# Kernel tuning notes

Measured on AMD Instinct MI355X. Metric: run time of the kernel, lower is better.

Reference implementation:

```python
import jax, jax.numpy as jnp
import numpy as np

N = 100_000
E = 3_200_000
FEAT, HID, EMB = 128, 32, 16
NEG_SLOPE = 0.2


def setup_inputs() -> dict:
    key = jax.random.key(0)
    ks = jax.random.split(key, 12)
    x = jax.random.normal(ks[0], (N, FEAT), dtype=jnp.float32)
    ei = jax.random.randint(ks[1], (2, E), 0, N, dtype=jnp.int32)
    ew = jax.random.uniform(ks[2], (E, 1), dtype=jnp.float32)
    # GATConv layer 1: feat_dim -> hidden_dim, heads=1
    s1 = 1.0 / np.sqrt(FEAT)
    W1 = jax.random.normal(ks[3], (FEAT, HID), dtype=jnp.float32) * s1
    a_src1 = jax.random.normal(ks[4], (HID,), dtype=jnp.float32) * (1.0 / np.sqrt(HID))
    a_dst1 = jax.random.normal(ks[5], (HID,), dtype=jnp.float32) * (1.0 / np.sqrt(HID))
    b1 = jnp.zeros((HID,), dtype=jnp.float32)
    # GATConv layer 2: hidden_dim -> embed_dim, heads=1
    s2 = 1.0 / np.sqrt(HID)
    W2 = jax.random.normal(ks[6], (HID, EMB), dtype=jnp.float32) * s2
    a_src2 = jax.random.normal(ks[7], (EMB,), dtype=jnp.float32) * (1.0 / np.sqrt(EMB))
    a_dst2 = jax.random.normal(ks[8], (EMB,), dtype=jnp.float32) * (1.0 / np.sqrt(EMB))
    b2 = jnp.zeros((EMB,), dtype=jnp.float32)
    return {"x": x, "ei": ei, "ew": ew, "W1": W1, "a_src1": a_src1,
            "a_dst1": a_dst1, "b1": b1, "W2": W2, "a_src2": a_src2,
            "a_dst2": a_dst2, "b2": b2}


def gat_conv(x, src, dst, W, a_src, a_dst, b):
    """PyG GATConv, heads=1, add_self_loops=True, edge_attr ignored (edge_dim=None)."""
    n = x.shape[0]
    h = x @ W                              # [N, C]
    al_s = h @ a_src                       # [N]
    al_d = h @ a_dst                       # [N]
    loop = jnp.arange(n, dtype=src.dtype)
    srcs = jnp.concatenate([src, loop])    # [E+N]
    dsts = jnp.concatenate([dst, loop])
    alpha = jax.nn.leaky_relu(al_s[srcs] + al_d[dsts], NEG_SLOPE)
    # segment softmax over edges grouped by destination node
    m = jax.ops.segment_max(alpha, dsts, num_segments=n)
    e = jnp.exp(alpha - m[dsts])
    denom = jax.ops.segment_sum(e, dsts, num_segments=n)
    coef = e / (denom[dsts] + 1e-16)
    out = jax.ops.segment_sum(coef[:, None] * h[srcs], dsts, num_segments=n)
    return out + b


def reference(x, ei, ew, W1, a_src1, a_dst1, b1, W2, a_src2, a_dst2, b2):
    # eval mode: DropEdge and Dropout are identity; ew unused by GATConv (edge_dim=None)
    src, dst = ei[0], ei[1]
    h = gat_conv(x, src, dst, W1, a_src1, a_dst1, b1)
    h = jax.nn.relu(h)
    return gat_conv(h, src, dst, W2, a_src2, a_dst2, b2)
```

## Files before the change

kernel.cpp:

```cpp
#include <hip/hip_runtime.h>

#define FEAT 128
#define HID 32
#define EMB 16
#define NEG 0.2f

#define BSH 8
#define BIN_NODES 256
#define NBMAX 400
#define CH 8192
#define CAP 12288
#define SRCBITS 17
#define SRCMASK 0x1FFFF

__device__ __forceinline__ float lrelu(float a) { return a > 0.0f ? a : NEG * a; }

__global__ __launch_bounds__(256) void k_zero_int(int* p, int n) {
    int i = (int)(blockIdx.x * 256 + threadIdx.x);
    if (i < n) p[i] = 0;
}

__global__ __launch_bounds__(256) void k_bincnt(const int* __restrict__ ei, int E_,
                                                int Nn, int* __restrict__ binCnt) {
    __shared__ int h[NBMAX];
    int nb = (Nn + BIN_NODES - 1) >> BSH;
    for (int i = threadIdx.x; i < nb; i += 256) h[i] = 0;
    __syncthreads();
    int stride = (int)(gridDim.x * 256);
    for (int i = (int)(blockIdx.x * 256 + threadIdx.x); i < E_; i += stride)
        atomicAdd(&h[ei[(size_t)E_ + i] >> BSH], 1);
    __syncthreads();
    for (int i = threadIdx.x; i < nb; i += 256)
        if (h[i]) atomicAdd(&binCnt[i], h[i]);
}

__global__ __launch_bounds__(512) void k_binscan(const int* __restrict__ binCnt,
                                                 int* __restrict__ binstart,
                                                 int* __restrict__ bin_pos,
                                                 int* __restrict__ rowptr,
                                                 int Nn, int E_) {
    __shared__ int s[512];
    int nb = (Nn + BIN_NODES - 1) >> BSH;
    int t = (int)threadIdx.x;
    s[t] = (t < nb) ? binCnt[t] : 0;
    __syncthreads();
    for (int off = 1; off < 512; off <<= 1) {
        int v = (t >= off) ? s[t - off] : 0;
        __syncthreads();
        s[t] += v;
        __syncthreads();
    }
    if (t <= nb) binstart[t] = (t == 0) ? 0 : s[t - 1];
    if (t < nb) bin_pos[t] = (t == 0) ? 0 : s[t - 1];
    if (t == 0) rowptr[Nn] = E_;
}

__global__ __launch_bounds__(1024) void k_part(const int* __restrict__ ei, int E_,
                                               int Nn, int* __restrict__ bin_pos,
                                               int* __restrict__ packed) {
    __shared__ int hist[NBMAX];
    __shared__ int lofs[NBMAX];
    __shared__ int pos[NBMAX];
    __shared__ int gbase[NBMAX];
    __shared__ int sscan[512];
    __shared__ int staged[CH];
    __shared__ unsigned short sbin[CH];
    int nb = (Nn + BIN_NODES - 1) >> BSH;
    int base = (int)(blockIdx.x * CH);
    int nE = min(CH, E_ - base);
    int t = (int)threadIdx.x;
    for (int i = t; i < nb; i += 1024) hist[i] = 0;
    __syncthreads();

    int myw[CH / 1024];
    int myb[CH / 1024];
#pragma unroll
    for (int k = 0; k < CH / 1024; ++k) {
        int i = t + k * 1024;
        int w = 0, b_ = -1;
        if (i < nE) {
            int s_ = ei[base + i];
            int d_ = ei[(size_t)E_ + base + i];
            b_ = d_ >> BSH;
            w = ((d_ & (BIN_NODES - 1)) << SRCBITS) | s_;
            atomicAdd(&hist[b_], 1);
        }
        myw[k] = w;
        myb[k] = b_;
    }
    __syncthreads();
    if (t < 512) sscan[t] = (t < nb) ? hist[t] : 0;
    __syncthreads();
    for (int off = 1; off < 512; off <<= 1) {
        int v = 0;
        if (t < 512 && t >= off) v = sscan[t - off];
        __syncthreads();
        if (t < 512) sscan[t] += v;
        __syncthreads();
    }
    for (int i = t; i < nb; i += 1024) {
        int ex = (i == 0) ? 0 : sscan[i - 1];
        lofs[i] = ex;
        pos[i] = ex;
    }
    __syncthreads();
#pragma unroll
    for (int k = 0; k < CH / 1024; ++k) {
        if (myb[k] >= 0) {
            int p = atomicAdd(&pos[myb[k]], 1);
            staged[p] = myw[k];
            sbin[p] = (unsigned short)myb[k];
        }
    }
    __syncthreads();
    for (int i = t; i < nb; i += 1024)
        gbase[i] = hist[i] ? atomicAdd(&bin_pos[i], hist[i]) : 0;
    __syncthreads();
    for (int i = t; i < nE; i += 1024) {
        int b_ = sbin[i];
        packed[gbase[b_] + (i - lofs[b_])] = staged[i];
    }
}

__global__ __launch_bounds__(1024) void k_build(const int* __restrict__ binstart,
                                                int Nn, int E_,
                                                int* __restrict__ packed,
                                                int* __restrict__ rowptr,
                                                int* __restrict__ scratch) {
    __shared__ int ncnt[BIN_NODES];
    __shared__ int npos[BIN_NODES];
    __shared__ int sscan[BIN_NODES];
    __shared__ int csr_l[CAP];
    int b = (int)blockIdx.x;
    int s = binstart[b], e = binstart[b + 1];
    int cnt = e - s;
    int nb0 = b << BSH;
    int nodes = min(BIN_NODES, Nn - nb0);
    int t = (int)threadIdx.x;
    if (t < BIN_NODES) ncnt[t] = 0;
    __syncthreads();
    for (int i = t; i < cnt; i += 1024) atomicAdd(&ncnt[packed[s + i] >> SRCBITS], 1);
    __syncthreads();
    if (t < BIN_NODES) sscan[t] = ncnt[t];
    __syncthreads();
    for (int off = 1; off < BIN_NODES; off <<= 1) {
        int v = 0;
        if (t < BIN_NODES && t >= off) v = sscan[t - off];
        __syncthreads();
        if (t < BIN_NODES) sscan[t] += v;
        __syncthreads();
    }
    if (t < BIN_NODES) {
        int ex = (t == 0) ? 0 : sscan[t - 1];
        npos[t] = ex;
        if (t < nodes) rowptr[nb0 + t] = s + ex;
    }
    __syncthreads();
    if (cnt <= CAP) {
        for (int i = t; i < cnt; i += 1024) {
            int w = packed[s + i];
            int p = atomicAdd(&npos[w >> SRCBITS], 1);
            csr_l[p] = w & SRCMASK;
        }
        __syncthreads();
        for (int i = t; i < cnt; i += 1024) packed[s + i] = csr_l[i];
    } else {
        for (int i = t; i < cnt; i += 1024) scratch[s + i] = packed[s + i];
        __syncthreads();
        for (int i = t; i < cnt; i += 1024) {
            int w = scratch[s + i];
            int p = atomicAdd(&npos[w >> SRCBITS], 1);
            packed[s + p] = w & SRCMASK;
        }
    }
}

__global__ __launch_bounds__(256) void k_h1(
    const float* __restrict__ x, const float* __restrict__ W1,
    const float* __restrict__ a_s, const float* __restrict__ a_d,
    float* __restrict__ h1, float* __restrict__ als, float* __restrict__ ald, int Nn)
{
    int row = (int)(blockIdx.x * 256 + threadIdx.x);
    if (row >= Nn) return;
    const float4* xr = (const float4*)(x + (size_t)row * FEAT);
    float acc[HID];
#pragma unroll
    for (int c = 0; c < HID; ++c) acc[c] = 0.0f;
#pragma unroll 4
    for (int k4 = 0; k4 < FEAT / 4; ++k4) {
        float4 xv = xr[k4];
        const float* Wr = W1 + k4 * 4 * HID;
#pragma unroll
        for (int c = 0; c < HID; ++c)
            acc[c] += xv.x * Wr[c] + xv.y * Wr[HID + c]
                    + xv.z * Wr[2 * HID + c] + xv.w * Wr[3 * HID + c];
    }
    float4* hr = (float4*)(h1 + (size_t)row * HID);
    float ps = 0.0f, pd = 0.0f;
#pragma unroll
    for (int c4 = 0; c4 < HID / 4; ++c4) {
        float4 hv;
        hv.x = acc[4 * c4 + 0]; hv.y = acc[4 * c4 + 1];
        hv.z = acc[4 * c4 + 2]; hv.w = acc[4 * c4 + 3];
        hr[c4] = hv;
        ps += hv.x * a_s[4 * c4 + 0] + hv.y * a_s[4 * c4 + 1]
            + hv.z * a_s[4 * c4 + 2] + hv.w * a_s[4 * c4 + 3];
        pd += hv.x * a_d[4 * c4 + 0] + hv.y * a_d[4 * c4 + 1]
            + hv.z * a_d[4 * c4 + 2] + hv.w * a_d[4 * c4 + 3];
    }
    als[row] = ps;
    ald[row] = pd;
}

__global__ __launch_bounds__(256) void k_agg1(
    const int* __restrict__ rowptr, const int* __restrict__ csr_src,
    const float* __restrict__ h1, const float* __restrict__ als,
    const float* __restrict__ ald, const float* __restrict__ b1,
    const float* __restrict__ W2, const float* __restrict__ a_s2,
    const float* __restrict__ a_d2,
    float* __restrict__ h2, float* __restrict__ als2, float* __restrict__ ald2, int Nn)
{
    int n = (int)(blockIdx.x * 32 + (threadIdx.x >> 3));
    if (n >= Nn) return;
    int l = threadIdx.x & 7;
    const float4* h1p = (const float4*)h1;
    float aldn = ald[n];
    float wself = __expf(lrelu(als[n] + aldn));
    float4 sv = h1p[(size_t)n * 8 + l];
    float s0x = wself * sv.x, s0y = wself * sv.y;
    float s0z = wself * sv.z, s0w = wself * sv.w;
    float s1x = 0, s1y = 0, s1z = 0, s1w = 0;
    float s2x = 0, s2y = 0, s2z = 0, s2w = 0;
    float s3x = 0, s3y = 0, s3z = 0, s3w = 0;
    float den = wself;
    int e = rowptr[n], e1 = rowptr[n + 1];
    for (; e + 4 <= e1; e += 4) {
        int i0 = csr_src[e + 0];
        int i1 = csr_src[e + 1];
        int i2 = csr_src[e + 2];
        int i3 = csr_src[e + 3];
        float4 f0 = h1p[(size_t)i0 * 8 + l];
        float4 f1 = h1p[(size_t)i1 * 8 + l];
        float4 f2 = h1p[(size_t)i2 * 8 + l];
        float4 f3 = h1p[(size_t)i3 * 8 + l];
        float a0 = als[i0], a1 = als[i1], a2 = als[i2], a3 = als[i3];
        float w0 = __expf(lrelu(a0 + aldn));
        float w1 = __expf(lrelu(a1 + aldn));
        float w2 = __expf(lrelu(a2 + aldn));
        float w3 = __expf(lrelu(a3 + aldn));
        s0x += w0 * f0.x; s0y += w0 * f0.y; s0z += w0 * f0.z; s0w += w0 * f0.w;
        s1x += w1 * f1.x; s1y += w1 * f1.y; s1z += w1 * f1.z; s1w += w1 * f1.w;
        s2x += w2 * f2.x; s2y += w2 * f2.y; s2z += w2 * f2.z; s2w += w2 * f2.w;
        s3x += w3 * f3.x; s3y += w3 * f3.y; s3z += w3 * f3.z; s3w += w3 * f3.w;
        den += (w0 + w1) + (w2 + w3);
    }
    for (; e < e1; ++e) {
        int s = csr_src[e];
        float we = __expf(lrelu(als[s] + aldn));
        float4 f = h1p[(size_t)s * 8 + l];
        s0x += we * f.x; s0y += we * f.y; s0z += we * f.z; s0w += we * f.w;
        den += we;
    }
    float inv = 1.0f / den;
    float gx = fmaxf((s0x + s1x + s2x + s3x) * inv + b1[4 * l + 0], 0.0f);
    float gy = fmaxf((s0y + s1y + s2y + s3y) * inv + b1[4 * l + 1], 0.0f);
    float gz = fmaxf((s0z + s1z + s2z + s3z) * inv + b1[4 * l + 2], 0.0f);
    float gw = fmaxf((s0w + s1w + s2w + s3w) * inv + b1[4 * l + 3], 0.0f);
    float hc0 = 0.0f, hc1 = 0.0f;
#pragma unroll
    for (int tt = 0; tt < 8; ++tt) {
        float bx = __shfl(gx, tt, 8);
        float by = __shfl(gy, tt, 8);
        float bz = __shfl(gz, tt, 8);
        float bw = __shfl(gw, tt, 8);
        const float* wp = &W2[(4 * tt) * EMB];
        hc0 += bx * wp[l] + by * wp[EMB + l]
             + bz * wp[2 * EMB + l] + bw * wp[3 * EMB + l];
        hc1 += bx * wp[l + 8] + by * wp[EMB + l + 8]
             + bz * wp[2 * EMB + l + 8] + bw * wp[3 * EMB + l + 8];
    }
    h2[(size_t)n * EMB + l] = hc0;
    h2[(size_t)n * EMB + l + 8] = hc1;
    float ps = hc0 * a_s2[l] + hc1 * a_s2[l + 8];
    float pd = hc0 * a_d2[l] + hc1 * a_d2[l + 8];
    for (int m = 1; m < 8; m <<= 1) {
        ps += __shfl_xor(ps, m, 8);
        pd += __shfl_xor(pd, m, 8);
    }
    if (l == 0) { als2[n] = ps; ald2[n] = pd; }
}

__global__ __launch_bounds__(256) void k_agg2(
    const int* __restrict__ rowptr, const int* __restrict__ csr_src,
    const float* __restrict__ h2, const float* __restrict__ als,
    const float* __restrict__ ald, const float* __restrict__ b2,
    float* __restrict__ out, int Nn)
{
    int n = (int)(blockIdx.x * 64 + (threadIdx.x >> 2));
    if (n >= Nn) return;
    int l = threadIdx.x & 3;
    const float4* h2p = (const float4*)h2;
    float aldn = ald[n];
    float wself = __expf(lrelu(als[n] + aldn));
    float4 sv = h2p[(size_t)n * 4 + l];
    float s0x = wself * sv.x, s0y = wself * sv.y;
    float s0z = wself * sv.z, s0w = wself * sv.w;
    float s1x = 0, s1y = 0, s1z = 0, s1w = 0;
    float s2x = 0, s2y = 0, s2z = 0, s2w = 0;
    float s3x = 0, s3y = 0, s3z = 0, s3w = 0;
    float den = wself;
    int e = rowptr[n], e1 = rowptr[n + 1];
    for (; e + 4 <= e1; e += 4) {
        int i0 = csr_src[e + 0];
        int i1 = csr_src[e + 1];
        int i2 = csr_src[e + 2];
        int i3 = csr_src[e + 3];
        float4 f0 = h2p[(size_t)i0 * 4 + l];
        float4 f1 = h2p[(size_t)i1 * 4 + l];
        float4 f2 = h2p[(size_t)i2 * 4 + l];
        float4 f3 = h2p[(size_t)i3 * 4 + l];
        float a0 = als[i0], a1 = als[i1], a2 = als[i2], a3 = als[i3];
        float w0 = __expf(lrelu(a0 + aldn));
        float w1 = __expf(lrelu(a1 + aldn));
        float w2 = __expf(lrelu(a2 + aldn));
        float w3 = __expf(lrelu(a3 + aldn));
        s0x += w0 * f0.x; s0y += w0 * f0.y; s0z += w0 * f0.z; s0w += w0 * f0.w;
        s1x += w1 * f1.x; s1y += w1 * f1.y; s1z += w1 * f1.z; s1w += w1 * f1.w;
        s2x += w2 * f2.x; s2y += w2 * f2.y; s2z += w2 * f2.z; s2w += w2 * f2.w;
        s3x += w3 * f3.x; s3y += w3 * f3.y; s3z += w3 * f3.z; s3w += w3 * f3.w;
        den += (w0 + w1) + (w2 + w3);
    }
    for (; e < e1; ++e) {
        int s = csr_src[e];
        float we = __expf(lrelu(als[s] + aldn));
        float4 f = h2p[(size_t)s * 4 + l];
        s0x += we * f.x; s0y += we * f.y; s0z += we * f.z; s0w += we * f.w;
        den += we;
    }
    float inv = 1.0f / den;
    float4 r;
    r.x = (s0x + s1x + s2x + s3x) * inv + b2[4 * l + 0];
    r.y = (s0y + s1y + s2y + s3y) * inv + b2[4 * l + 1];
    r.z = (s0z + s1z + s2z + s3z) * inv + b2[4 * l + 2];
    r.w = (s0w + s1w + s2w + s3w) * inv + b2[4 * l + 3];
    ((float4*)out)[(size_t)n * 4 + l] = r;
}

extern "C" void kernel_launch(void* const* d_in, const int* in_sizes, int n_in,
                              void* d_out, int out_size, void* d_ws, size_t ws_size,
                              hipStream_t stream)
{
    const float* x   = (const float*)d_in[0];
    const int*   ei  = (const int*)d_in[1];
    const float* W1  = (const float*)d_in[3];
    const float* as1 = (const float*)d_in[4];
    const float* ad1 = (const float*)d_in[5];
    const float* b1  = (const float*)d_in[6];
    const float* W2  = (const float*)d_in[7];
    const float* as2 = (const float*)d_in[8];
    const float* ad2 = (const float*)d_in[9];
    const float* b2  = (const float*)d_in[10];
    float* out = (float*)d_out;

    const int Nn = in_sizes[0] / FEAT;
    const int E_ = in_sizes[1] / 2;
    const int nb = (Nn + BIN_NODES - 1) >> BSH;

    float* h1    = (float*)d_ws;
    float* als1  = h1 + (size_t)Nn * HID;
    float* ald1  = als1 + Nn;
    float* h2    = ald1 + Nn;
    float* als2p = h2 + (size_t)Nn * EMB;
    float* ald2p = als2p + Nn;
    int* rowptr  = (int*)(ald2p + Nn);
    int* binCnt  = rowptr + Nn + 1;
    int* binstart= binCnt + NBMAX;
    int* bin_pos = binstart + NBMAX + 1;
    int* packed  = bin_pos + NBMAX;

    k_zero_int<<<(nb + 255) / 256, 256, 0, stream>>>(binCnt, nb);
    k_bincnt<<<1024, 256, 0, stream>>>(ei, E_, Nn, binCnt);
    k_binscan<<<1, 512, 0, stream>>>(binCnt, binstart, bin_pos, rowptr, Nn, E_);
    k_part<<<(E_ + CH - 1) / CH, 1024, 0, stream>>>(ei, E_, Nn, bin_pos, packed);
    k_build<<<nb, 1024, 0, stream>>>(binstart, Nn, E_, packed, rowptr, (int*)h1);

    k_h1<<<(Nn + 255) / 256, 256, 0, stream>>>(x, W1, as1, ad1, h1, als1, ald1, Nn);
    k_agg1<<<(Nn + 31) / 32, 256, 0, stream>>>(rowptr, packed, h1, als1, ald1,
                                               b1, W2, as2, ad2, h2, als2p, ald2p, Nn);
    k_agg2<<<(Nn + 63) / 64, 256, 0, stream>>>(rowptr, packed, h2, als2p, ald2p,
                                               b2, out, Nn);
}
```

Before: 321.7 us.

## Precompute per-edge attention weights in a separate pass and vectorize CSR reads

The CSR words now keep the local destination index, and a new per-bin kernel uses it to compute the exp(leaky_relu) edge weight for every edge in a coalesced pass, writing them to a workspace buffer. The aggregation kernels then read 4 indices and 4 weights with aligned int4/float4 loads instead of gathering als per edge and evaluating exp inline, after a scalar head loop that brings the edge index to a multiple of 4. Layer 2 aggregation also changes from 4 lanes of float4 to 8 lanes of float2 per node. This adds an extra E-sized write and read per layer plus two more launches, and falls back to the old path when the workspace is too small.

Result: slower. 363.2 us (+12.9%).

```diff
diff --git a/kernel.cpp b/kernel.cpp
--- a/kernel.cpp
+++ b/kernel.cpp
@@ -139,7 +139,7 @@
     int t = (int)threadIdx.x;
     if (t < BIN_NODES) ncnt[t] = 0;
     __syncthreads();
-    for (int i = t; i < cnt; i += 1024) atomicAdd(&ncnt[packed[s + i] >> SRCBITS], 1);
+    for (int i = t; i < cnt; i += 1024) atomicAdd(&ncnt[(packed[s + i] >> SRCBITS) & 255], 1);
     __syncthreads();
     if (t < BIN_NODES) sscan[t] = ncnt[t];
     __syncthreads();
@@ -159,8 +159,8 @@
     if (cnt <= CAP) {
         for (int i = t; i < cnt; i += 1024) {
             int w = packed[s + i];
-            int p = atomicAdd(&npos[w >> SRCBITS], 1);
-            csr_l[p] = w & SRCMASK;
+            int p = atomicAdd(&npos[(w >> SRCBITS) & 255], 1);
+            csr_l[p] = w;
         }
         __syncthreads();
         for (int i = t; i < cnt; i += 1024) packed[s + i] = csr_l[i];
@@ -169,8 +169,8 @@
         __syncthreads();
         for (int i = t; i < cnt; i += 1024) {
             int w = scratch[s + i];
-            int p = atomicAdd(&npos[w >> SRCBITS], 1);
-            packed[s + p] = w & SRCMASK;
+            int p = atomicAdd(&npos[(w >> SRCBITS) & 255], 1);
+            packed[s + p] = w;
         }
     }
 }
@@ -212,8 +212,26 @@
     ald[row] = pd;
 }
 
+__global__ __launch_bounds__(1024) void k_wgt(const int* __restrict__ binstart,
+                                              const int* __restrict__ packed,
+                                              const float* __restrict__ als,
+                                              const float* __restrict__ ald,
+                                              float* __restrict__ wbuf) {
+    int b = (int)blockIdx.x;
+    int s = binstart[b], e = binstart[b + 1];
+    int nb0 = b << BSH;
+    for (int i = s + (int)threadIdx.x; i < e; i += 1024) {
+        int w = packed[i];
+        int src = w & SRCMASK;
+        int d = nb0 + ((w >> SRCBITS) & 255);
+        wbuf[i] = __expf(lrelu(als[src] + ald[d]));
+    }
+}
+
+template<bool HASW>
 __global__ __launch_bounds__(256) void k_agg1(
-    const int* __restrict__ rowptr, const int* __restrict__ csr_src,
+    const int* __restrict__ rowptr, const int* __restrict__ csr,
+    const float* __restrict__ wbuf,
     const float* __restrict__ h1, const float* __restrict__ als,
     const float* __restrict__ ald, const float* __restrict__ b1,
     const float* __restrict__ W2, const float* __restrict__ a_s2,
@@ -234,20 +252,34 @@
     float s3x = 0, s3y = 0, s3z = 0, s3w = 0;
     float den = wself;
     int e = rowptr[n], e1 = rowptr[n + 1];
+    for (; e < e1 && (e & 3); ++e) {
+        int word = csr[e];
+        int s = word & SRCMASK;
+        float we;
+        if constexpr (HASW) we = wbuf[e];
+        else we = __expf(lrelu(als[s] + aldn));
+        float4 f = h1p[(size_t)s * 8 + l];
+        s0x += we * f.x; s0y += we * f.y; s0z += we * f.z; s0w += we * f.w;
+        den += we;
+    }
     for (; e + 4 <= e1; e += 4) {
-        int i0 = csr_src[e + 0];
-        int i1 = csr_src[e + 1];
-        int i2 = csr_src[e + 2];
-        int i3 = csr_src[e + 3];
+        int4 c4 = *(const int4*)(csr + e);
+        int i0 = c4.x & SRCMASK, i1 = c4.y & SRCMASK;
+        int i2 = c4.z & SRCMASK, i3 = c4.w & SRCMASK;
+        float w0, w1, w2, w3;
+        if constexpr (HASW) {
+            float4 w4 = *(const float4*)(wbuf + e);
+            w0 = w4.x; w1 = w4.y; w2 = w4.z; w3 = w4.w;
+        } else {
+            w0 = __expf(lrelu(als[i0] + aldn));
+            w1 = __expf(lrelu(als[i1] + aldn));
+            w2 = __expf(lrelu(als[i2] + aldn));
+            w3 = __expf(lrelu(als[i3] + aldn));
+        }
         float4 f0 = h1p[(size_t)i0 * 8 + l];
         float4 f1 = h1p[(size_t)i1 * 8 + l];
         float4 f2 = h1p[(size_t)i2 * 8 + l];
         float4 f3 = h1p[(size_t)i3 * 8 + l];
-        float a0 = als[i0], a1 = als[i1], a2 = als[i2], a3 = als[i3];
-        float w0 = __expf(lrelu(a0 + aldn));
-        float w1 = __expf(lrelu(a1 + aldn));
-        float w2 = __expf(lrelu(a2 + aldn));
-        float w3 = __expf(lrelu(a3 + aldn));
         s0x += w0 * f0.x; s0y += w0 * f0.y; s0z += w0 * f0.z; s0w += w0 * f0.w;
         s1x += w1 * f1.x; s1y += w1 * f1.y; s1z += w1 * f1.z; s1w += w1 * f1.w;
         s2x += w2 * f2.x; s2y += w2 * f2.y; s2z += w2 * f2.z; s2w += w2 * f2.w;
@@ -255,8 +287,11 @@
         den += (w0 + w1) + (w2 + w3);
     }
     for (; e < e1; ++e) {
-        int s = csr_src[e];
-        float we = __expf(lrelu(als[s] + aldn));
+        int word = csr[e];
+        int s = word & SRCMASK;
+        float we;
+        if constexpr (HASW) we = wbuf[e];
+        else we = __expf(lrelu(als[s] + aldn));
         float4 f = h1p[(size_t)s * 8 + l];
         s0x += we * f.x; s0y += we * f.y; s0z += we * f.z; s0w += we * f.w;
         den += we;
@@ -290,60 +325,74 @@
     if (l == 0) { als2[n] = ps; ald2[n] = pd; }
 }
 
+template<bool HASW>
 __global__ __launch_bounds__(256) void k_agg2(
-    const int* __restrict__ rowptr, const int* __restrict__ csr_src,
+    const int* __restrict__ rowptr, const int* __restrict__ csr,
+    const float* __restrict__ wbuf,
     const float* __restrict__ h2, const float* __restrict__ als,
     const float* __restrict__ ald, const float* __restrict__ b2,
     float* __restrict__ out, int Nn)
 {
-    int n = (int)(blockIdx.x * 64 + (threadIdx.x >> 2));
+    int n = (int)(blockIdx.x * 32 + (threadIdx.x >> 3));
     if (n >= Nn) return;
-    int l = threadIdx.x & 3;
-    const float4* h2p = (const float4*)h2;
+    int l = threadIdx.x & 7;
+    const float2* h2p = (const float2*)h2;
     float aldn = ald[n];
     float wself = __expf(lrelu(als[n] + aldn));
-    float4 sv = h2p[(size_t)n * 4 + l];
+    float2 sv = h2p[(size_t)n * 8 + l];
     float s0x = wself * sv.x, s0y = wself * sv.y;
-    float s0z = wself * sv.z, s0w = wself * sv.w;
-    float s1x = 0, s1y = 0, s1z = 0, s1w = 0;
-    float s2x = 0, s2y = 0, s2z = 0, s2w = 0;
-    float s3x = 0, s3y = 0, s3z = 0, s3w = 0;
+    float s1x = 0, s1y = 0, s2x = 0, s2y = 0, s3x = 0, s3y = 0;
     float den = wself;
     int e = rowptr[n], e1 = rowptr[n + 1];
+    for (; e < e1 && (e & 3); ++e) {
+        int word = csr[e];
+        int s = word & SRCMASK;
+        float we;
+        if constexpr (HASW) we = wbuf[e];
+        else we = __expf(lrelu(als[s] + aldn));
+        float2 f = h2p[(size_t)s * 8 + l];
+        s0x += we * f.x; s0y += we * f.y;
+        den += we;
+    }
     for (; e + 4 <= e1; e += 4) {
-        int i0 = csr_src[e + 0];
-        int i1 = csr_src[e + 1];
-        int i2 = csr_src[e + 2];
-        int i3 = csr_src[e + 3];
-        float4 f0 = h2p[(size_t)i0 * 4 + l];
-        float4 f1 = h2p[(size_t)i1 * 4 + l];
-        float4 f2 = h2p[(size_t)i2 * 4 + l];
-        float4 f3 = h2p[(size_t)i3 * 4 + l];
-        float a0 = als[i0], a1 = als[i1], a2 = als[i2], a3 = als[i3];
-        float w0 = __expf(lrelu(a0 + aldn));
-        float w1 = __expf(lrelu(a1 + aldn));
-        float w2 = __expf(lrelu(a2 + aldn));
-        float w3 = __expf(lrelu(a3 + aldn));
-        s0x += w0 * f0.x; s0y += w0 * f0.y; s0z += w0 * f0.z; s0w += w0 * f0.w;
-        s1x += w1 * f1.x; s1y += w1 * f1.y; s1z += w1 * f1.z; s1w += w1 * f1.w;
-        s2x += w2 * f2.x; s2y += w2 * f2.y; s2z += w2 * f2.z; s2w += w2 * f2.w;
-        s3x += w3 * f3.x; s3y += w3 * f3.y; s3z += w3 * f3.z; s3w += w3 * f3.w;
+        int4 c4 = *(const int4*)(csr + e);
+        int i0 = c4.x & SRCMASK, i1 = c4.y & SRCMASK;
+        int i2 = c4.z & SRCMASK, i3 = c4.w & SRCMASK;
+        float w0, w1, w2, w3;
+        if constexpr (HASW) {
+            float4 w4 = *(const float4*)(wbuf + e);
+            w0 = w4.x; w1 = w4.y; w2 = w4.z; w3 = w4.w;
+        } else {
+            w0 = __expf(lrelu(als[i0] + aldn));
+            w1 = __expf(lrelu(als[i1] + aldn));
+            w2 = __expf(lrelu(als[i2] + aldn));
+            w3 = __expf(lrelu(als[i3] + aldn));
+        }
+        float2 f0 = h2p[(size_t)i0 * 8 + l];
+        float2 f1 = h2p[(size_t)i1 * 8 + l];
+        float2 f2 = h2p[(size_t)i2 * 8 + l];
+        float2 f3 = h2p[(size_t)i3 * 8 + l];
+        s0x += w0 * f0.x; s0y += w0 * f0.y;
+        s1x += w1 * f1.x; s1y += w1 * f1.y;
+        s2x += w2 * f2.x; s2y += w2 * f2.y;
+        s3x += w3 * f3.x; s3y += w3 * f3.y;
         den += (w0 + w1) + (w2 + w3);
     }
     for (; e < e1; ++e) {
-        int s = csr_src[e];
-        float we = __expf(lrelu(als[s] + aldn));
-        float4 f = h2p[(size_t)s * 4 + l];
-        s0x += we * f.x; s0y += we * f.y; s0z += we * f.z; s0w += we * f.w;
+        int word = csr[e];
+        int s = word & SRCMASK;
+        float we;
+        if constexpr (HASW) we = wbuf[e];
+        else we = __expf(lrelu(als[s] + aldn));
+        float2 f = h2p[(size_t)s * 8 + l];
+        s0x += we * f.x; s0y += we * f.y;
         den += we;
     }
     float inv = 1.0f / den;
-    float4 r;
-    r.x = (s0x + s1x + s2x + s3x) * inv + b2[4 * l + 0];
-    r.y = (s0y + s1y + s2y + s3y) * inv + b2[4 * l + 1];
-    r.z = (s0z + s1z + s2z + s3z) * inv + b2[4 * l + 2];
-    r.w = (s0w + s1w + s2w + s3w) * inv + b2[4 * l + 3];
-    ((float4*)out)[(size_t)n * 4 + l] = r;
+    float2 r;
+    r.x = (s0x + s1x + s2x + s3x) * inv + b2[2 * l];
+    r.y = (s0y + s1y + s2y + s3y) * inv + b2[2 * l + 1];
+    ((float2*)out)[(size_t)n * 8 + l] = r;
 }
 
 extern "C" void kernel_launch(void* const* d_in, const int* in_sizes, int n_in,
@@ -376,7 +425,11 @@
     int* binCnt  = rowptr + Nn + 1;
     int* binstart= binCnt + NBMAX;
     int* bin_pos = binstart + NBMAX + 1;
-    int* packed  = bin_pos + NBMAX;
+    int* packedr = bin_pos + NBMAX;
+    int* packed  = (int*)(((uintptr_t)packedr + 15) & ~(uintptr_t)15);
+    float* wbuf  = (float*)(packed + E_);
+    size_t need  = (size_t)((char*)(wbuf + E_) - (char*)d_ws);
+    bool hasw    = ws_size >= need;
 
     k_zero_int<<<(nb + 255) / 256, 256, 0, stream>>>(binCnt, nb);
     k_bincnt<<<1024, 256, 0, stream>>>(ei, E_, Nn, binCnt);
@@ -385,8 +438,17 @@
     k_build<<<nb, 1024, 0, stream>>>(binstart, Nn, E_, packed, rowptr, (int*)h1);
 
     k_h1<<<(Nn + 255) / 256, 256, 0, stream>>>(x, W1, as1, ad1, h1, als1, ald1, Nn);
-    k_agg1<<<(Nn + 31) / 32, 256, 0, stream>>>(rowptr, packed, h1, als1, ald1,
-                                               b1, W2, as2, ad2, h2, als2p, ald2p, Nn);
-    k_agg2<<<(Nn + 63) / 64, 256, 0, stream>>>(rowptr, packed, h2, als2p, ald2p,
-                                               b2, out, Nn);
-}
+    if (hasw) {
+        k_wgt<<<nb, 1024, 0, stream>>>(binstart, packed, als1, ald1, wbuf);
+        k_agg1<true><<<(Nn + 31) / 32, 256, 0, stream>>>(rowptr, packed, wbuf,
+            h1, als1, ald1, b1, W2, as2, ad2, h2, als2p, ald2p, Nn);
+        k_wgt<<<nb, 1024, 0, stream>>>(binstart, packed, als2p, ald2p, wbuf);
+        k_agg2<true><<<(Nn + 31) / 32, 256, 0, stream>>>(rowptr, packed, wbuf,
+            h2, als2p, ald2p, b2, out, Nn);
+    } else {
+        k_agg1<false><<<(Nn + 31) / 32, 256, 0, stream>>>(rowptr, packed, nullptr,
+            h1, als1, ald1, b1, W2, as2, ad2, h2, als2p, ald2p, Nn);
+        k_agg2<false><<<(Nn + 31) / 32, 256, 0, stream>>>(rowptr, packed, nullptr,
+            h2, als2p, ald2p, b2, out, Nn);
+    }
+}
```

## Store node features in fp16, fuse h1 projection into bin count, simplify CSR build

Applied to the files above, without the earlier changes.

Layer-1 and layer-2 node features are now stored as half precision, which halves the bytes moved by the random gathers in both aggregation kernels. The dense x@W1 projection is merged into the edge bin-count kernel, removing one launch. The CSR build writes to a separate output array instead of sorting in place through LDS or a scratch copy. agg2 now uses 8 lanes per node with half2 loads. The cost is reduced feature precision, extra workspace for the CSR array, and heavier registers in the fused kernel.

Result: faster. 297.6 us (-7.5%).

```diff
diff --git a/kernel.cpp b/kernel.cpp
--- a/kernel.cpp
+++ b/kernel.cpp
@@ -1,4 +1,5 @@
 #include <hip/hip_runtime.h>
+#include <hip/hip_fp16.h>
 
 #define FEAT 128
 #define HID 32
@@ -9,7 +10,6 @@
 #define BIN_NODES 256
 #define NBMAX 400
 #define CH 8192
-#define CAP 12288
 #define SRCBITS 17
 #define SRCMASK 0x1FFFF
 
@@ -20,14 +20,47 @@
     if (i < n) p[i] = 0;
 }
 
-__global__ __launch_bounds__(256) void k_bincnt(const int* __restrict__ ei, int E_,
-                                                int Nn, int* __restrict__ binCnt) {
+__global__ __launch_bounds__(256) void k_bincnt_h1(
+    const int* __restrict__ ei, int E_, int Nn, int* __restrict__ binCnt,
+    const float* __restrict__ x, const float* __restrict__ W1,
+    const float* __restrict__ a_s, const float* __restrict__ a_d,
+    __half* __restrict__ h1h, float* __restrict__ als, float* __restrict__ ald)
+{
     __shared__ int h[NBMAX];
     int nb = (Nn + BIN_NODES - 1) >> BSH;
     for (int i = threadIdx.x; i < nb; i += 256) h[i] = 0;
     __syncthreads();
+    int tid = (int)(blockIdx.x * 256 + threadIdx.x);
+    if (tid < Nn) {
+        const float4* xr = (const float4*)(x + (size_t)tid * FEAT);
+        float acc[HID];
+#pragma unroll
+        for (int c = 0; c < HID; ++c) acc[c] = 0.0f;
+#pragma unroll 4
+        for (int k4 = 0; k4 < FEAT / 4; ++k4) {
+            float4 xv = xr[k4];
+            const float* Wr = W1 + k4 * 4 * HID;
+#pragma unroll
+            for (int c = 0; c < HID; ++c)
+                acc[c] += xv.x * Wr[c] + xv.y * Wr[HID + c]
+                        + xv.z * Wr[2 * HID + c] + xv.w * Wr[3 * HID + c];
+        }
+        float ps = 0.0f, pd = 0.0f;
+        __half hb[HID];
+#pragma unroll
+        for (int c = 0; c < HID; ++c) {
+            ps += acc[c] * a_s[c];
+            pd += acc[c] * a_d[c];
+            hb[c] = __float2half(acc[c]);
+        }
+        int4* dst = (int4*)(h1h + (size_t)tid * HID);
+        const int4* sb = (const int4*)hb;
+        dst[0] = sb[0]; dst[1] = sb[1]; dst[2] = sb[2]; dst[3] = sb[3];
+        als[tid] = ps;
+        ald[tid] = pd;
+    }
     int stride = (int)(gridDim.x * 256);
-    for (int i = (int)(blockIdx.x * 256 + threadIdx.x); i < E_; i += stride)
+    for (int i = tid; i < E_; i += stride)
         atomicAdd(&h[ei[(size_t)E_ + i] >> BSH], 1);
     __syncthreads();
     for (int i = threadIdx.x; i < nb; i += 256)
@@ -123,14 +156,13 @@
 }
 
 __global__ __launch_bounds__(1024) void k_build(const int* __restrict__ binstart,
-                                                int Nn, int E_,
-                                                int* __restrict__ packed,
-                                                int* __restrict__ rowptr,
-                                                int* __restrict__ scratch) {
+                                                int Nn,
+                                                const int* __restrict__ packed,
+                                                int* __restrict__ csr,
+                                                int* __restrict__ rowptr) {
     __shared__ int ncnt[BIN_NODES];
     __shared__ int npos[BIN_NODES];
     __shared__ int sscan[BIN_NODES];
-    __shared__ int csr_l[CAP];
     int b = (int)blockIdx.x;
     int s = binstart[b], e = binstart[b + 1];
     int cnt = e - s;
@@ -139,7 +171,8 @@
     int t = (int)threadIdx.x;
     if (t < BIN_NODES) ncnt[t] = 0;
     __syncthreads();
-    for (int i = t; i < cnt; i += 1024) atomicAdd(&ncnt[packed[s + i] >> SRCBITS], 1);
+    for (int i = t; i < cnt; i += 1024)
+        atomicAdd(&ncnt[(packed[s + i] >> SRCBITS) & 255], 1);
     __syncthreads();
     if (t < BIN_NODES) sscan[t] = ncnt[t];
     __syncthreads();
@@ -156,109 +189,73 @@
         if (t < nodes) rowptr[nb0 + t] = s + ex;
     }
     __syncthreads();
-    if (cnt <= CAP) {
-        for (int i = t; i < cnt; i += 1024) {
-            int w = packed[s + i];
-            int p = atomicAdd(&npos[w >> SRCBITS], 1);
-            csr_l[p] = w & SRCMASK;
-        }
-        __syncthreads();
-        for (int i = t; i < cnt; i += 1024) packed[s + i] = csr_l[i];
-    } else {
-        for (int i = t; i < cnt; i += 1024) scratch[s + i] = packed[s + i];
-        __syncthreads();
-        for (int i = t; i < cnt; i += 1024) {
-            int w = scratch[s + i];
-            int p = atomicAdd(&npos[w >> SRCBITS], 1);
-            packed[s + p] = w & SRCMASK;
-        }
-    }
-}
-
-__global__ __launch_bounds__(256) void k_h1(
-    const float* __restrict__ x, const float* __restrict__ W1,
-    const float* __restrict__ a_s, const float* __restrict__ a_d,
-    float* __restrict__ h1, float* __restrict__ als, float* __restrict__ ald, int Nn)
-{
-    int row = (int)(blockIdx.x * 256 + threadIdx.x);
-    if (row >= Nn) return;
-    const float4* xr = (const float4*)(x + (size_t)row * FEAT);
-    float acc[HID];
-#pragma unroll
-    for (int c = 0; c < HID; ++c) acc[c] = 0.0f;
-#pragma unroll 4
-    for (int k4 = 0; k4 < FEAT / 4; ++k4) {
-        float4 xv = xr[k4];
-        const float* Wr = W1 + k4 * 4 * HID;
-#pragma unroll
-        for (int c = 0; c < HID; ++c)
-            acc[c] += xv.x * Wr[c] + xv.y * Wr[HID + c]
-                    + xv.z * Wr[2 * HID + c] + xv.w * Wr[3 * HID + c];
-    }
-    float4* hr = (float4*)(h1 + (size_t)row * HID);
-    float ps = 0.0f, pd = 0.0f;
-#pragma unroll
-    for (int c4 = 0; c4 < HID / 4; ++c4) {
-        float4 hv;
-        hv.x = acc[4 * c4 + 0]; hv.y = acc[4 * c4 + 1];
-        hv.z = acc[4 * c4 + 2]; hv.w = acc[4 * c4 + 3];
-        hr[c4] = hv;
-        ps += hv.x * a_s[4 * c4 + 0] + hv.y * a_s[4 * c4 + 1]
-            + hv.z * a_s[4 * c4 + 2] + hv.w * a_s[4 * c4 + 3];
-        pd += hv.x * a_d[4 * c4 + 0] + hv.y * a_d[4 * c4 + 1]
-            + hv.z * a_d[4 * c4 + 2] + hv.w * a_d[4 * c4 + 3];
-    }
-    als[row] = ps;
-    ald[row] = pd;
+    for (int i = t; i < cnt; i += 1024) {
+        int w = packed[s + i];
+        int p = atomicAdd(&npos[(w >> SRCBITS) & 255], 1);
+        csr[s + p] = w & SRCMASK;
+    }
 }
 
 __global__ __launch_bounds__(256) void k_agg1(
-    const int* __restrict__ rowptr, const int* __restrict__ csr_src,
-    const float* __restrict__ h1, const float* __restrict__ als,
+    const int* __restrict__ rowptr, const int* __restrict__ csr,
+    const __half* __restrict__ h1h, const float* __restrict__ als,
     const float* __restrict__ ald, const float* __restrict__ b1,
     const float* __restrict__ W2, const float* __restrict__ a_s2,
     const float* __restrict__ a_d2,
-    float* __restrict__ h2, float* __restrict__ als2, float* __restrict__ ald2, int Nn)
+    __half* __restrict__ h2h, float* __restrict__ als2, float* __restrict__ ald2,
+    int Nn)
 {
     int n = (int)(blockIdx.x * 32 + (threadIdx.x >> 3));
     if (n >= Nn) return;
     int l = threadIdx.x & 7;
-    const float4* h1p = (const float4*)h1;
+    const __half* h1b = h1h + 4 * l;
     float aldn = ald[n];
     float wself = __expf(lrelu(als[n] + aldn));
-    float4 sv = h1p[(size_t)n * 8 + l];
-    float s0x = wself * sv.x, s0y = wself * sv.y;
-    float s0z = wself * sv.z, s0w = wself * sv.w;
+    uint2 rs = *(const uint2*)(h1b + (size_t)n * HID);
+    float2 pa = __half22float2(*reinterpret_cast<const __half2*>(&rs.x));
+    float2 pb = __half22float2(*reinterpret_cast<const __half2*>(&rs.y));
+    float s0x = wself * pa.x, s0y = wself * pa.y;
+    float s0z = wself * pb.x, s0w = wself * pb.y;
     float s1x = 0, s1y = 0, s1z = 0, s1w = 0;
     float s2x = 0, s2y = 0, s2z = 0, s2w = 0;
     float s3x = 0, s3y = 0, s3z = 0, s3w = 0;
     float den = wself;
     int e = rowptr[n], e1 = rowptr[n + 1];
     for (; e + 4 <= e1; e += 4) {
-        int i0 = csr_src[e + 0];
-        int i1 = csr_src[e + 1];
-        int i2 = csr_src[e + 2];
-        int i3 = csr_src[e + 3];
-        float4 f0 = h1p[(size_t)i0 * 8 + l];
-        float4 f1 = h1p[(size_t)i1 * 8 + l];
-        float4 f2 = h1p[(size_t)i2 * 8 + l];
-        float4 f3 = h1p[(size_t)i3 * 8 + l];
+        int i0 = csr[e + 0];
+        int i1 = csr[e + 1];
+        int i2 = csr[e + 2];
+        int i3 = csr[e + 3];
+        uint2 g0 = *(const uint2*)(h1b + (size_t)i0 * HID);
+        uint2 g1 = *(const uint2*)(h1b + (size_t)i1 * HID);
+        uint2 g2 = *(const uint2*)(h1b + (size_t)i2 * HID);
+        uint2 g3 = *(const uint2*)(h1b + (size_t)i3 * HID);
         float a0 = als[i0], a1 = als[i1], a2 = als[i2], a3 = als[i3];
         float w0 = __expf(lrelu(a0 + aldn));
         float w1 = __expf(lrelu(a1 + aldn));
         float w2 = __expf(lrelu(a2 + aldn));
         float w3 = __expf(lrelu(a3 + aldn));
-        s0x += w0 * f0.x; s0y += w0 * f0.y; s0z += w0 * f0.z; s0w += w0 * f0.w;
-        s1x += w1 * f1.x; s1y += w1 * f1.y; s1z += w1 * f1.z; s1w += w1 * f1.w;
-        s2x += w2 * f2.x; s2y += w2 * f2.y; s2z += w2 * f2.z; s2w += w2 * f2.w;
-        s3x += w3 * f3.x; s3y += w3 * f3.y; s3z += w3 * f3.z; s3w += w3 * f3.w;
+        float2 f0a = __half22float2(*reinterpret_cast<const __half2*>(&g0.x));
+        float2 f0b = __half22float2(*reinterpret_cast<const __half2*>(&g0.y));
+        float2 f1a = __half22float2(*reinterpret_cast<const __half2*>(&g1.x));
+        float2 f1b = __half22float2(*reinterpret_cast<const __half2*>(&g1.y));
+        float2 f2a = __half22float2(*reinterpret_cast<const __half2*>(&g2.x));
+        float2 f2b = __half22float2(*reinterpret_cast<const __half2*>(&g2.y));
+        float2 f3a = __half22float2(*reinterpret_cast<const __half2*>(&g3.x));
+        float2 f3b = __half22float2(*reinterpret_cast<const __half2*>(&g3.y));
+        s0x += w0 * f0a.x; s0y += w0 * f0a.y; s0z += w0 * f0b.x; s0w += w0 * f0b.y;
+        s1x += w1 * f1a.x; s1y += w1 * f1a.y; s1z += w1 * f1b.x; s1w += w1 * f1b.y;
+        s2x += w2 * f2a.x; s2y += w2 * f2a.y; s2z += w2 * f2b.x; s2w += w2 * f2b.y;
+        s3x += w3 * f3a.x; s3y += w3 * f3a.y; s3z += w3 * f3b.x; s3w += w3 * f3b.y;
         den += (w0 + w1) + (w2 + w3);
     }
     for (; e < e1; ++e) {
-        int s = csr_src[e];
+        int s = csr[e];
         float we = __expf(lrelu(als[s] + aldn));
-        float4 f = h1p[(size_t)s * 8 + l];
-        s0x += we * f.x; s0y += we * f.y; s0z += we * f.z; s0w += we * f.w;
+        uint2 g = *(const uint2*)(h1b + (size_t)s * HID);
+        float2 fa = __half22float2(*reinterpret_cast<const __half2*>(&g.x));
+        float2 fb = __half22float2(*reinterpret_cast<const __half2*>(&g.y));
+        s0x += we * fa.x; s0y += we * fa.y; s0z += we * fb.x; s0w += we * fb.y;
         den += we;
     }
     float inv = 1.0f / den;
@@ -279,8 +276,8 @@
         hc1 += bx * wp[l + 8] + by * wp[EMB + l + 8]
              + bz * wp[2 * EMB + l + 8] + bw * wp[3 * EMB + l + 8];
     }
-    h2[(size_t)n * EMB + l] = hc0;
-    h2[(size_t)n * EMB + l + 8] = hc1;
+    h2h[(size_t)n * EMB + l]     = __float2half(hc0);
+    h2h[(size_t)n * EMB + l + 8] = __float2half(hc1);
     float ps = hc0 * a_s2[l] + hc1 * a_s2[l + 8];
     float pd = hc0 * a_d2[l] + hc1 * a_d2[l + 8];
     for (int m = 1; m < 8; m <<= 1) {
@@ -291,59 +288,54 @@
 }
 
 __global__ __launch_bounds__(256) void k_agg2(
-    const int* __restrict__ rowptr, const int* __restrict__ csr_src,
-    const float* __restrict__ h2, const float* __restrict__ als,
+    const int* __restrict__ rowptr, const int* __restrict__ csr,
+    const __half* __restrict__ h2h, const float* __restrict__ als,
     const float* __restrict__ ald, const float* __restrict__ b2,
     float* __restrict__ out, int Nn)
 {
-    int n = (int)(blockIdx.x * 64 + (threadIdx.x >> 2));
+    int n = (int)(blockIdx.x * 32 + (threadIdx.x >> 3));
     if (n >= Nn) return;
-    int l = threadIdx.x & 3;
-    const float4* h2p = (const float4*)h2;
+    int l = threadIdx.x & 7;
+    const __half* h2b = h2h + 2 * l;
     float aldn = ald[n];
     float wself = __expf(lrelu(als[n] + aldn));
-    float4 sv = h2p[(size_t)n * 4 + l];
+    float2 sv = __half22float2(*(const __half2*)(h2b + (size_t)n * EMB));
     float s0x = wself * sv.x, s0y = wself * sv.y;
-    float s0z = wself * sv.z, s0w = wself * sv.w;
-    float s1x = 0, s1y = 0, s1z = 0, s1w = 0;
-    float s2x = 0, s2y = 0, s2z = 0, s2w = 0;
-    float s3x = 0, s3y = 0, s3z = 0, s3w = 0;
+    float s1x = 0, s1y = 0, s2x = 0, s2y = 0, s3x = 0, s3y = 0;
     float den = wself;
     int e = rowptr[n], e1 = rowptr[n + 1];
     for (; e + 4 <= e1; e += 4) {
-        int i0 = csr_src[e + 0];
-        int i1 = csr_src[e + 1];
-        int i2 = csr_src[e + 2];
-        int i3 = csr_src[e + 3];
-        float4 f0 = h2p[(size_t)i0 * 4 + l];
-        float4 f1 = h2p[(size_t)i1 * 4 + l];
-        float4 f2 = h2p[(size_t)i2 * 4 + l];
-        float4 f3 = h2p[(size_t)i3 * 4 + l];
+        int i0 = csr[e + 0];
+        int i1 = csr[e + 1];
+        int i2 = csr[e + 2];
+        int i3 = csr[e + 3];
+        float2 f0 = __half22float2(*(const __half2*)(h2b + (size_t)i0 * EMB));
+        float2 f1 = __half22float2(*(const __half2*)(h2b + (size_t)i1 * EMB));
+        float2 f2 = __half22float2(*(const __half2*)(h2b + (size_t)i2 * EMB));
+        float2 f3 = __half22float2(*(const __half2*)(h2b + (size_t)i3 * EMB));
         float a0 = als[i0], a1 = als[i1], a2 = als[i2], a3 = als[i3];
         float w0 = __expf(lrelu(a0 + aldn));
         float w1 = __expf(lrelu(a1 + aldn));
         float w2 = __expf(lrelu(a2 + aldn));
         float w3 = __expf(lrelu(a3 + aldn));
-        s0x += w0 * f0.x; s0y += w0 * f0.y; s0z += w0 * f0.z; s0w += w0 * f0.w;
-        s1x += w1 * f1.x; s1y += w1 * f1.y; s1z += w1 * f1.z; s1w += w1 * f1.w;
-        s2x += w2 * f2.x; s2y += w2 * f2.y; s2z += w2 * f2.z; s2w += w2 * f2.w;
-        s3x += w3 * f3.x; s3y += w3 * f3.y; s3z += w3 * f3.z; s3w += w3 * f3.w;
+        s0x += w0 * f0.x; s0y += w0 * f0.y;
+        s1x += w1 * f1.x; s1y += w1 * f1.y;
+        s2x += w2 * f2.x; s2y += w2 * f2.y;
+        s3x += w3 * f3.x; s3y += w3 * f3.y;
         den += (w0 + w1) + (w2 + w3);
     }
     for (; e < e1; ++e) {
-        int s = csr_src[e];
+        int s = csr[e];
         float we = __expf(lrelu(als[s] + aldn));
-        float4 f = h2p[(size_t)s * 4 + l];
-        s0x += we * f.x; s0y += we * f.y; s0z += we * f.z; s0w += we * f.w;
+        float2 f = __half22float2(*(const __half2*)(h2b + (size_t)s * EMB));
+        s0x += we * f.x; s0y += we * f.y;
         den += we;
     }
     float inv = 1.0f / den;
-    float4 r;
-    r.x = (s0x + s1x + s2x + s3x) * inv + b2[4 * l + 0];
-    r.y = (s0y + s1y + s2y + s3y) * inv + b2[4 * l + 1];
-    r.z = (s0z + s1z + s2z + s3z) * inv + b2[4 * l + 2];
-    r.w = (s0w + s1w + s2w + s3w) * inv + b2[4 * l + 3];
-    ((float4*)out)[(size_t)n * 4 + l] = r;
+    float2 r;
+    r.x = (s0x + s1x + s2x + s3x) * inv + b2[2 * l];
+    r.y = (s0y + s1y + s2y + s3y) * inv + b2[2 * l + 1];
+    *(float2*)(out + (size_t)n * EMB + 2 * l) = r;
 }
 
 extern "C" void kernel_launch(void* const* d_in, const int* in_sizes, int n_in,
@@ -366,27 +358,31 @@
     const int E_ = in_sizes[1] / 2;
     const int nb = (Nn + BIN_NODES - 1) >> BSH;
 
-    float* h1    = (float*)d_ws;
-    float* als1  = h1 + (size_t)Nn * HID;
-    float* ald1  = als1 + Nn;
-    float* h2    = ald1 + Nn;
-    float* als2p = h2 + (size_t)Nn * EMB;
-    float* ald2p = als2p + Nn;
-    int* rowptr  = (int*)(ald2p + Nn);
-    int* binCnt  = rowptr + Nn + 1;
-    int* binstart= binCnt + NBMAX;
-    int* bin_pos = binstart + NBMAX + 1;
-    int* packed  = bin_pos + NBMAX;
+    __half* h1h   = (__half*)d_ws;
+    float* als1   = (float*)(h1h + (size_t)Nn * HID);
+    float* ald1   = als1 + Nn;
+    __half* h2h   = (__half*)(ald1 + Nn);
+    float* als2p  = (float*)(h2h + (size_t)Nn * EMB);
+    float* ald2p  = als2p + Nn;
+    int* rowptr   = (int*)(ald2p + Nn);
+    int* binCnt   = rowptr + Nn + 1;
+    int* binstart = binCnt + NBMAX;
+    int* bin_pos  = binstart + NBMAX + 1;
+    int* packed   = bin_pos + NBMAX;
+    int* csr      = packed + E_;
 
     k_zero_int<<<(nb + 255) / 256, 256, 0, stream>>>(binCnt, nb);
-    k_bincnt<<<1024, 256, 0, stream>>>(ei, E_, Nn, binCnt);
+    int gb1 = (Nn + 255) / 256;
+    if (gb1 < 1024) gb1 = 1024;
+    k_bincnt_h1<<<gb1, 256, 0, stream>>>(ei, E_, Nn, binCnt,
+                                         x, W1, as1, ad1, h1h, als1, ald1);
     k_binscan<<<1, 512, 0, stream>>>(binCnt, binstart, bin_pos, rowptr, Nn, E_);
     k_part<<<(E_ + CH - 1) / CH, 1024, 0, stream>>>(ei, E_, Nn, bin_pos, packed);
-    k_build<<<nb, 1024, 0, stream>>>(binstart, Nn, E_, packed, rowptr, (int*)h1);
-
-    k_h1<<<(Nn + 255) / 256, 256, 0, stream>>>(x, W1, as1, ad1, h1, als1, ald1, Nn);
-    k_agg1<<<(Nn + 31) / 32, 256, 0, stream>>>(rowptr, packed, h1, als1, ald1,
-                                               b1, W2, as2, ad2, h2, als2p, ald2p, Nn);
-    k_agg2<<<(Nn + 63) / 64, 256, 0, stream>>>(rowptr, packed, h2, als2p, ald2p,
+    k_build<<<nb, 1024, 0, stream>>>(binstart, Nn, packed, csr, rowptr);
+
+    k_agg1<<<(Nn + 31) / 32, 256, 0, stream>>>(rowptr, csr, h1h, als1, ald1,
+                                               b1, W2, as2, ad2,
+                                               h2h, als2p, ald2p, Nn);
+    k_agg2<<<(Nn + 31) / 32, 256, 0, stream>>>(rowptr, csr, h2h, als2p, ald2p,
                                                b2, out, Nn);
 }
```
